# Optimization experiments

Measured on AMD Instinct MI355X. Metric: run time of the kernel, lower is better.

Reference implementation:

```python
import math
import jax, jax.numpy as jnp
import numpy as np

B, QL, CL, D, H = 4, 2048, 2048, 512, 8  # batch, q_len, c_len, hidden/query/context dim, heads
A = D // H
SCALE = 1.0 / math.sqrt(D)
FILL = -100000.0


def setup_inputs() -> dict:
    key = jax.random.key(0)
    ks = jax.random.split(key, 6)
    query = jax.random.normal(ks[0], (B, QL, D), dtype=jnp.float32)
    context = jax.random.normal(ks[1], (B, CL, D), dtype=jnp.float32)
    mask = jax.random.randint(ks[2], (B, CL, H), 0, 2).astype(bool)
    Wq = (jax.random.normal(ks[3], (D, D)) * 0.02).astype(jnp.float32)    # Q: query_dim -> hidden_dim (no bias)
    Wkv = (jax.random.normal(ks[4], (D, 2 * D)) * 0.02).astype(jnp.float32)  # KV: context_dim -> 2*hidden_dim
    Wout = (jax.random.normal(ks[5], (D, D)) * 0.02).astype(jnp.float32)  # out: hidden_dim -> context_dim
    return {"query": query, "context": context, "mask": mask, "Wq": Wq, "Wkv": Wkv, "Wout": Wout}


def reference(query, context, mask, Wq, Wkv, Wout):
    b, q_len, _ = query.shape
    c_len = context.shape[1]
    q = (query @ Wq).reshape(b, q_len, H, A)
    kv = context @ Wkv
    k = kv[..., :D].reshape(b, c_len, H, A)
    v = kv[..., D:].reshape(b, c_len, H, A)
    # [b, q, k, h] scores
    scores = jnp.einsum('bqha,bkha->bqkh', q, k)
    # mask.unsqueeze(1): [b, 1, c_len, h]; apply_mask == where(mask, FILL, x)
    scores = jnp.where(mask[:, None, :, :], FILL, scores)
    attn_weights = jax.nn.softmax(scores * SCALE, axis=2)
    # NOTE: faithful to original torch einsum 'bqkh,bvha->bqha' (k and v are
    # independent summed indices, as in the source code).
    attn = jnp.einsum('bqkh,bvha->bqha', attn_weights, v)
    attn = attn.reshape(b, q_len, D)
    return attn @ Wout
```

## Files before the change

### kernel.cpp

```cpp
#include <hip/hip_runtime.h>

#define BATCH 4
#define QLEN 2048
#define CLEN 2048
#define DIM 512
#define NBLK1 1024
#define CPB 256
#define RPC 8


__global__ __launch_bounds__(256) void k1_partial(const float* __restrict__ ctx,
                                                  float4* __restrict__ partial) {
    __shared__ float4 red[256];
    const int blk = blockIdx.x, t = threadIdx.x;
    const int b = blk >> 8, ch = blk & 255;
    const int rg = t >> 7, f4 = t & 127;
    const float4* src = reinterpret_cast<const float4*>(ctx)
                      + (size_t)(b * CLEN + ch * RPC) * (DIM / 4);
    float4 s = make_float4(0.f, 0.f, 0.f, 0.f);
#pragma unroll
    for (int i = 0; i < 4; ++i) {
        float4 x = src[(size_t)(rg + 2 * i) * (DIM / 4) + f4];
        s.x += x.x; s.y += x.y; s.z += x.z; s.w += x.w;
    }
    red[t] = s;
    __syncthreads();
    if (t < 128) {
        float4 a = red[t], c = red[t + 128];
        partial[(size_t)blk * (DIM / 4) + t] =
            make_float4(a.x + c.x, a.y + c.y, a.z + c.z, a.w + c.w);
    }
}

__global__ __launch_bounds__(256) void k2_reduce(const float4* __restrict__ partial,
                                                 float4* __restrict__ csum) {
    __shared__ float4 red[256];
    const int blk = blockIdx.x, t = threadIdx.x;
    const int b = blk >> 7, f4g = blk & 127;
    red[t] = partial[(size_t)(b * CPB + t) * (DIM / 4) + f4g];
    __syncthreads();
#pragma unroll
    for (int s = 128; s > 0; s >>= 1) {
        if (t < s) {
            float4 a = red[t], c = red[t + s];
            red[t] = make_float4(a.x + c.x, a.y + c.y, a.z + c.z, a.w + c.w);
        }
        __syncthreads();
    }
    if (t == 0) csum[b * (DIM / 4) + f4g] = red[0];
}

__global__ __launch_bounds__(256) void k3_vsum(const float* __restrict__ csum,
                                               const float* __restrict__ Wkv,
                                               float* __restrict__ vsum) {
    __shared__ float cs[DIM];
    __shared__ float red[256];
    const int blk = blockIdx.x, t = threadIdx.x;
    const int b = blk >> 5, eg = blk & 31;
    for (int j = t; j < DIM; j += 256) cs[j] = csum[b * DIM + j];
    __syncthreads();
    const int el = t & 15, dg = t >> 4;
    const int e = eg * 16 + el;
    const float* w = Wkv + (size_t)dg * (2 * DIM) + DIM + e;
    float s = 0.f;
#pragma unroll
    for (int i = 0; i < 32; ++i)
        s += cs[i * 16 + dg] * w[(size_t)i * 16 * (2 * DIM)];
    red[t] = s;
    __syncthreads();
#pragma unroll
    for (int st = 128; st >= 16; st >>= 1) {
        if (t < st) red[t] += red[t + st];
        __syncthreads();
    }
    if (t < 16) vsum[b * DIM + eg * 16 + t] = red[t];
}

__global__ __launch_bounds__(256) void k4_orow(const float* __restrict__ vsum,
                                               const float* __restrict__ Wout,
                                               float* __restrict__ orow) {
    __shared__ float vs[DIM];
    __shared__ float red[256];
    const int blk = blockIdx.x, t = threadIdx.x;
    const int b = blk >> 5, fg = blk & 31;
    for (int j = t; j < DIM; j += 256) vs[j] = vsum[b * DIM + j];
    __syncthreads();
    const int fl = t & 15, eg2 = t >> 4;
    const int f = fg * 16 + fl;
    const float* w = Wout + (size_t)eg2 * DIM + f;
    float s = 0.f;
#pragma unroll
    for (int i = 0; i < 32; ++i)
        s += vs[i * 16 + eg2] * w[(size_t)i * 16 * DIM];
    red[t] = s;
    __syncthreads();
#pragma unroll
    for (int st = 128; st >= 16; st >>= 1) {
        if (t < st) red[t] += red[t + st];
        __syncthreads();
    }
    if (t < 16) orow[b * DIM + fg * 16 + t] = red[t];
}

__global__ __launch_bounds__(256) void k5_bcast(const float4* __restrict__ orow4,
                                                float4* __restrict__ out) {
    const int blk = blockIdx.x, t = threadIdx.x;
    const int b = blk >> 8, qg = blk & 255;
    const int rg = t >> 7, f4 = t & 127;
    const float4 val = orow4[b * (DIM / 4) + f4];
    float4* dst = out + (size_t)(b * QLEN + qg * RPC) * (DIM / 4);
#pragma unroll
    for (int i = 0; i < 4; ++i)
        dst[(size_t)(rg + 2 * i) * (DIM / 4) + f4] = val;
}

extern "C" void kernel_launch(void* const* d_in, const int* in_sizes, int n_in,
                              void* d_out, int out_size, void* d_ws, size_t ws_size,
                              hipStream_t stream) {
    const float* ctx  = (const float*)d_in[1];
    const float* Wkv  = (const float*)d_in[4];
    const float* Wout = (const float*)d_in[5];
    float* ws = (float*)d_ws;
    float* partial = ws;
    float* csum    = partial + (size_t)NBLK1 * DIM;
    float* vsum    = csum + BATCH * DIM;
    float* orow    = vsum + BATCH * DIM;

    k1_partial<<<NBLK1, 256, 0, stream>>>(ctx, (float4*)partial);
    k2_reduce<<<512, 256, 0, stream>>>((const float4*)partial, (float4*)csum);
    k3_vsum<<<128, 256, 0, stream>>>(csum, Wkv, vsum);
    k4_orow<<<128, 256, 0, stream>>>(vsum, Wout, orow);
    k5_bcast<<<NBLK1, 256, 0, stream>>>((const float4*)orow, (float4*)d_out);
}
```

Before: 26.70 us.

## Fuse context-sum reduce and both weight GEMVs into one middle kernel

Merges the partial-sum reduction, the V projection and the output projection into a single kernel with 32 blocks, each handling one batch and one 64-wide slice of V. The per-slice output contributions are written to a small buffer and summed inside the broadcast kernel. The first kernel now reduces 16 rows per block, which halves the partial buffer. This removes two kernel launches and their dependency gaps, but the fused middle stage runs on only 32 blocks, and each block redundantly re-reduces the 128 partial rows for its batch.

Result: no change. 26.75 us (+0.2%).

```diff
diff --git a/kernel.cpp b/kernel.cpp
--- a/kernel.cpp
+++ b/kernel.cpp
@@ -4,22 +4,23 @@
 #define QLEN 2048
 #define CLEN 2048
 #define DIM 512
-#define NBLK1 1024
-#define CPB 256
-#define RPC 8
+#define NBLK1 512
+#define CPB 128
+#define RPC 16
+#define NSL 8
 
 
 __global__ __launch_bounds__(256) void k1_partial(const float* __restrict__ ctx,
                                                   float4* __restrict__ partial) {
     __shared__ float4 red[256];
     const int blk = blockIdx.x, t = threadIdx.x;
-    const int b = blk >> 8, ch = blk & 255;
+    const int b = blk >> 7, ch = blk & 127;
     const int rg = t >> 7, f4 = t & 127;
     const float4* src = reinterpret_cast<const float4*>(ctx)
                       + (size_t)(b * CLEN + ch * RPC) * (DIM / 4);
     float4 s = make_float4(0.f, 0.f, 0.f, 0.f);
 #pragma unroll
-    for (int i = 0; i < 4; ++i) {
+    for (int i = 0; i < 8; ++i) {
         float4 x = src[(size_t)(rg + 2 * i) * (DIM / 4) + f4];
         s.x += x.x; s.y += x.y; s.z += x.z; s.w += x.w;
     }
@@ -32,86 +33,78 @@
     }
 }
 
-__global__ __launch_bounds__(256) void k2_reduce(const float4* __restrict__ partial,
-                                                 float4* __restrict__ csum) {
+__global__ __launch_bounds__(256) void k2_middle(const float4* __restrict__ partial,
+                                                 const float* __restrict__ Wkv,
+                                                 const float* __restrict__ Wout,
+                                                 float* __restrict__ opart) {
     __shared__ float4 red[256];
+    __shared__ float cs[DIM];
+    __shared__ float vl[256];
+    __shared__ float vslice[64];
     const int blk = blockIdx.x, t = threadIdx.x;
-    const int b = blk >> 7, f4g = blk & 127;
-    red[t] = partial[(size_t)(b * CPB + t) * (DIM / 4) + f4g];
+    const int b1 = blk >> 3, sl = blk & 7;
+
+    {
+        const int g = t & 127, h = t >> 7;
+        const float4* p = partial + (size_t)(b1 * CPB + h * 64) * (DIM / 4) + g;
+        float4 s = make_float4(0.f, 0.f, 0.f, 0.f);
+#pragma unroll 16
+        for (int j = 0; j < 64; ++j) {
+            float4 x = p[(size_t)j * (DIM / 4)];
+            s.x += x.x; s.y += x.y; s.z += x.z; s.w += x.w;
+        }
+        red[t] = s;
+    }
     __syncthreads();
+    if (t < 128) {
+        float4 a = red[t], c = red[t + 128];
+        reinterpret_cast<float4*>(cs)[t] =
+            make_float4(a.x + c.x, a.y + c.y, a.z + c.z, a.w + c.w);
+    }
+    __syncthreads();
+
+    {
+        const int el = t & 63, dg = t >> 6;
+        const float* w = Wkv + (size_t)(dg * 128) * (2 * DIM) + DIM + sl * 64 + el;
+        float s = 0.f;
+#pragma unroll 8
+        for (int d0 = 0; d0 < 128; ++d0)
+            s += cs[dg * 128 + d0] * w[(size_t)d0 * (2 * DIM)];
+        vl[t] = s;
+    }
+    __syncthreads();
+    if (t < 64) vslice[t] = vl[t] + vl[t + 64] + vl[t + 128] + vl[t + 192];
+    __syncthreads();
+
+    {
 #pragma unroll
-    for (int s = 128; s > 0; s >>= 1) {
-        if (t < s) {
-            float4 a = red[t], c = red[t + s];
-            red[t] = make_float4(a.x + c.x, a.y + c.y, a.z + c.z, a.w + c.w);
+        for (int half = 0; half < 2; ++half) {
+            const int f = half * 256 + t;
+            const float* w = Wout + (size_t)(sl * 64) * DIM + f;
+            float s = 0.f;
+#pragma unroll 8
+            for (int e0 = 0; e0 < 64; ++e0)
+                s += vslice[e0] * w[(size_t)e0 * DIM];
+            opart[(size_t)(sl * BATCH + b1) * DIM + f] = s;
         }
-        __syncthreads();
     }
-    if (t == 0) csum[b * (DIM / 4) + f4g] = red[0];
 }
 
-__global__ __launch_bounds__(256) void k3_vsum(const float* __restrict__ csum,
-                                               const float* __restrict__ Wkv,
-                                               float* __restrict__ vsum) {
-    __shared__ float cs[DIM];
-    __shared__ float red[256];
-    const int blk = blockIdx.x, t = threadIdx.x;
-    const int b = blk >> 5, eg = blk & 31;
-    for (int j = t; j < DIM; j += 256) cs[j] = csum[b * DIM + j];
-    __syncthreads();
-    const int el = t & 15, dg = t >> 4;
-    const int e = eg * 16 + el;
-    const float* w = Wkv + (size_t)dg * (2 * DIM) + DIM + e;
-    float s = 0.f;
-#pragma unroll
-    for (int i = 0; i < 32; ++i)
-        s += cs[i * 16 + dg] * w[(size_t)i * 16 * (2 * DIM)];
-    red[t] = s;
-    __syncthreads();
-#pragma unroll
-    for (int st = 128; st >= 16; st >>= 1) {
-        if (t < st) red[t] += red[t + st];
-        __syncthreads();
-    }
-    if (t < 16) vsum[b * DIM + eg * 16 + t] = red[t];
-}
-
-__global__ __launch_bounds__(256) void k4_orow(const float* __restrict__ vsum,
-                                               const float* __restrict__ Wout,
-                                               float* __restrict__ orow) {
-    __shared__ float vs[DIM];
-    __shared__ float red[256];
-    const int blk = blockIdx.x, t = threadIdx.x;
-    const int b = blk >> 5, fg = blk & 31;
-    for (int j = t; j < DIM; j += 256) vs[j] = vsum[b * DIM + j];
-    __syncthreads();
-    const int fl = t & 15, eg2 = t >> 4;
-    const int f = fg * 16 + fl;
-    const float* w = Wout + (size_t)eg2 * DIM + f;
-    float s = 0.f;
-#pragma unroll
-    for (int i = 0; i < 32; ++i)
-        s += vs[i * 16 + eg2] * w[(size_t)i * 16 * DIM];
-    red[t] = s;
-    __syncthreads();
-#pragma unroll
-    for (int st = 128; st >= 16; st >>= 1) {
-        if (t < st) red[t] += red[t + st];
-        __syncthreads();
-    }
-    if (t < 16) orow[b * DIM + fg * 16 + t] = red[t];
-}
-
-__global__ __launch_bounds__(256) void k5_bcast(const float4* __restrict__ orow4,
+__global__ __launch_bounds__(256) void k3_bcast(const float4* __restrict__ opart4,
                                                 float4* __restrict__ out) {
     const int blk = blockIdx.x, t = threadIdx.x;
     const int b = blk >> 8, qg = blk & 255;
     const int rg = t >> 7, f4 = t & 127;
-    const float4 val = orow4[b * (DIM / 4) + f4];
-    float4* dst = out + (size_t)(b * QLEN + qg * RPC) * (DIM / 4);
+    float4 v = make_float4(0.f, 0.f, 0.f, 0.f);
+#pragma unroll
+    for (int sl = 0; sl < NSL; ++sl) {
+        float4 x = opart4[(size_t)(sl * BATCH + b) * (DIM / 4) + f4];
+        v.x += x.x; v.y += x.y; v.z += x.z; v.w += x.w;
+    }
+    float4* dst = out + (size_t)(b * QLEN + qg * 8) * (DIM / 4);
 #pragma unroll
     for (int i = 0; i < 4; ++i)
-        dst[(size_t)(rg + 2 * i) * (DIM / 4) + f4] = val;
+        dst[(size_t)(rg + 2 * i) * (DIM / 4) + f4] = v;
 }
 
 extern "C" void kernel_launch(void* const* d_in, const int* in_sizes, int n_in,
@@ -122,13 +115,9 @@
     const float* Wout = (const float*)d_in[5];
     float* ws = (float*)d_ws;
     float* partial = ws;
-    float* csum    = partial + (size_t)NBLK1 * DIM;
-    float* vsum    = csum + BATCH * DIM;
-    float* orow    = vsum + BATCH * DIM;
+    float* opart   = partial + (size_t)NBLK1 * DIM;
 
     k1_partial<<<NBLK1, 256, 0, stream>>>(ctx, (float4*)partial);
-    k2_reduce<<<512, 256, 0, stream>>>((const float4*)partial, (float4*)csum);
-    k3_vsum<<<128, 256, 0, stream>>>(csum, Wkv, vsum);
-    k4_orow<<<128, 256, 0, stream>>>(vsum, Wout, orow);
-    k5_bcast<<<NBLK1, 256, 0, stream>>>((const float4*)orow, (float4*)d_out);
+    k2_middle<<<BATCH * NSL, 256, 0, stream>>>((const float4*)partial, Wkv, Wout, opart);
+    k3_bcast<<<BATCH * 256, 256, 0, stream>>>((const float4*)opart, (float4*)d_out);
 }
```
